# Kernel tuning notes

Hardware: AMD Instinct MI355X
Metric: run time of the kernel (lower is better)

The kernel has to match this reference:

```python
import jax, jax.numpy as jnp
import numpy as np

N_NODES = 50000
N_EDGES = 800000
IN_F = 128
HEADS = 4
OUT_F = 16  # per-head channels; concat output = HEADS*OUT_F = 64
NEG_SLOPE = 0.2


def setup_inputs() -> dict:
    key = jax.random.key(0)
    ks = jax.random.split(key, 9)
    x = jax.random.normal(ks[0], (N_NODES, IN_F), dtype=jnp.float32)
    edge_index = jax.random.randint(ks[1], (2, N_EDGES), 0, N_NODES, dtype=jnp.int64)
    edge_attr = jax.random.normal(ks[2], (N_EDGES, 1), dtype=jnp.float32)
    s = 1.0 / np.sqrt(IN_F)
    W = jax.random.normal(ks[3], (IN_F, HEADS * OUT_F), dtype=jnp.float32) * s
    W_edge = jax.random.normal(ks[4], (1, HEADS * OUT_F), dtype=jnp.float32)
    att_src = jax.random.normal(ks[5], (HEADS, OUT_F), dtype=jnp.float32) * s
    att_dst = jax.random.normal(ks[6], (HEADS, OUT_F), dtype=jnp.float32) * s
    att_edge = jax.random.normal(ks[7], (HEADS, OUT_F), dtype=jnp.float32) * s
    bias = jax.random.normal(ks[8], (HEADS * OUT_F,), dtype=jnp.float32) * 0.01
    return {"x": x, "edge_index": edge_index, "edge_attr": edge_attr,
            "W": W, "W_edge": W_edge, "att_src": att_src,
            "att_dst": att_dst, "att_edge": att_edge, "bias": bias}


def reference(x, edge_index, edge_attr, W, W_edge, att_src, att_dst, att_edge, bias):
    N = x.shape[0]
    H, C = att_src.shape
    src, dst = edge_index[0], edge_index[1]

    # add_self_loops with fill_value='mean': per-dst mean of incoming edge_attr
    deg = jax.ops.segment_sum(jnp.ones_like(edge_attr[:, 0]), dst, num_segments=N)
    ea_mean = jax.ops.segment_sum(edge_attr, dst, num_segments=N) / jnp.maximum(deg, 1.0)[:, None]
    loop = jnp.arange(N, dtype=src.dtype)
    src_f = jnp.concatenate([src, loop])   # [E+N]
    dst_f = jnp.concatenate([dst, loop])
    ea = jnp.concatenate([edge_attr, ea_mean], axis=0)  # [E+N, 1]

    # node transform + per-node attention logits
    xw = (x @ W).reshape(N, H, C)                 # [N,H,C]
    a_src = jnp.einsum('nhc,hc->nh', xw, att_src)  # [N,H]
    a_dst = jnp.einsum('nhc,hc->nh', xw, att_dst)

    # edge feature transform + edge logits
    ew = (ea @ W_edge).reshape(-1, H, C)           # [E+N,H,C]
    a_edge = jnp.einsum('ehc,hc->eh', ew, att_edge)

    # gather, LeakyReLU, segment softmax over incoming edges per dst node
    alpha = jax.nn.leaky_relu(a_src[src_f] + a_dst[dst_f] + a_edge, NEG_SLOPE)  # [E+N,H]
    amax = jax.ops.segment_max(alpha, dst_f, num_segments=N)                    # [N,H]
    ex = jnp.exp(alpha - amax[dst_f])
    denom = jax.ops.segment_sum(ex, dst_f, num_segments=N)
    att = ex / denom[dst_f]                                                     # [E+N,H]

    # weighted scatter-aggregate of source messages
    msg = xw[src_f] * att[:, :, None]                       # [E+N,H,C]
    out = jax.ops.segment_sum(msg, dst_f, num_segments=N)    # [N,H,C]
    out = out.reshape(N, H * C) + bias

    # batchnorm=Identity, dropout in eval mode; activation=relu
    return jax.nn.relu(out)
```

## Files before the change

### kernel.cpp

```cpp
#include <hip/hip_runtime.h>
#include <hip/hip_fp16.h>
#include <math.h>

#define NN 50000
#define NE 800000
#define INF_ 128
#define HEADS 4
#define OUTF 16
#define HC 64
#define NEG_SLOPE 0.2f
#define NBKT 196
#define CHA 4096
#define NBA ((NE + CHA - 1) / CHA)
#define XPAD 136

typedef _Float16 half8 __attribute__((ext_vector_type(8)));
typedef float f32x4 __attribute__((ext_vector_type(4)));

__device__ __forceinline__ unsigned short h2u(float f) {
    __half h = __float2half(f);
    return *(unsigned short*)&h;
}
__device__ __forceinline__ float u2f(unsigned short u) {
    __half h = *(__half*)&u;
    return __half2float(h);
}

__global__ __launch_bounds__(256) void k_xw(
    const float* __restrict__ x, const float* __restrict__ W,
    const float* __restrict__ att_src, const float* __restrict__ att_dst,
    unsigned short* __restrict__ xw16, unsigned short* __restrict__ a_src16,
    float* __restrict__ a_dst) {
    __shared__ _Float16 sxh[64][XPAD];
    __shared__ _Float16 sWT[64][XPAD];
    int t = threadIdx.x;
    int n0 = blockIdx.x * 64;
    for (int i = t; i < 64 * 32; i += 256) {
        int r = i >> 5, c4 = (i & 31) * 4;
        int n = n0 + r;
        float4 v = (n < NN) ? *(const float4*)&x[(size_t)n * INF_ + c4]
                            : make_float4(0.f, 0.f, 0.f, 0.f);
        sxh[r][c4 + 0] = (_Float16)v.x;
        sxh[r][c4 + 1] = (_Float16)v.y;
        sxh[r][c4 + 2] = (_Float16)v.z;
        sxh[r][c4 + 3] = (_Float16)v.w;
    }
    for (int i = t; i < INF_ * HC; i += 256) {
        int k = i >> 6, c = i & 63;
        sWT[c][k] = (_Float16)W[i];
    }
    __syncthreads();
    int w = t >> 6, l = t & 63;
    int lr = l & 15, kg = l >> 4;
    f32x4 acc0 = {0.f,0.f,0.f,0.f}, acc1 = acc0, acc2 = acc0, acc3 = acc0;
#pragma unroll
    for (int kk = 0; kk < 4; ++kk) {
        half8 a = *(half8*)&sxh[w * 16 + lr][kk * 32 + kg * 8];
        half8 b0 = *(half8*)&sWT[0 * 16 + lr][kk * 32 + kg * 8];
        half8 b1 = *(half8*)&sWT[1 * 16 + lr][kk * 32 + kg * 8];
        half8 b2 = *(half8*)&sWT[2 * 16 + lr][kk * 32 + kg * 8];
        half8 b3 = *(half8*)&sWT[3 * 16 + lr][kk * 32 + kg * 8];
        acc0 = __builtin_amdgcn_mfma_f32_16x16x32_f16(a, b0, acc0, 0, 0, 0);
        acc1 = __builtin_amdgcn_mfma_f32_16x16x32_f16(a, b1, acc1, 0, 0, 0);
        acc2 = __builtin_amdgcn_mfma_f32_16x16x32_f16(a, b2, acc2, 0, 0, 0);
        acc3 = __builtin_amdgcn_mfma_f32_16x16x32_f16(a, b3, acc3, 0, 0, 0);
    }
    float attS[4], attD[4];
#pragma unroll
    for (int ct = 0; ct < 4; ++ct) {
        attS[ct] = att_src[ct * 16 + lr];
        attD[ct] = att_dst[ct * 16 + lr];
    }
    int rbase = n0 + w * 16 + kg * 4;
    f32x4 accs[4] = {acc0, acc1, acc2, acc3};
#pragma unroll
    for (int ct = 0; ct < 4; ++ct) {
#pragma unroll
        for (int j = 0; j < 4; ++j) {
            float c = accs[ct][j];
            int node = rbase + j;
            if (node < NN)
                xw16[(size_t)node * HC + ct * 16 + lr] = h2u(c);
            float vs = c * attS[ct];
            float vd = c * attD[ct];
#pragma unroll
            for (int m = 1; m < 16; m <<= 1) {
                vs += __shfl_xor(vs, m);
                vd += __shfl_xor(vd, m);
            }
            if (lr == 0 && node < NN) {
                a_src16[node * HEADS + ct] = h2u(vs);
                a_dst[node * HEADS + ct] = vd;
            }
        }
    }
}

__global__ __launch_bounds__(256) void k_coarse(const int* __restrict__ ei,
                                                int* __restrict__ ccnt) {
    __shared__ int lh[NBKT];
    int t = threadIdx.x;
    for (int i = t; i < NBKT; i += 256) lh[i] = 0;
    __syncthreads();
    for (int i = blockIdx.x * 256 + t; i < NE; i += gridDim.x * 256)
        atomicAdd(&lh[ei[NE + i] >> 8], 1);
    __syncthreads();
    for (int i = t; i < NBKT; i += 256)
        if (lh[i]) atomicAdd(&ccnt[i], lh[i]);
}

__global__ void k_scanb(const int* __restrict__ ccnt, int* __restrict__ boff,
                        int* __restrict__ ccur) {
    __shared__ int sd[256];
    int t = threadIdx.x;
    int v = (t < NBKT) ? ccnt[t] : 0;
    sd[t] = v; __syncthreads();
    for (int o = 1; o < 256; o <<= 1) {
        int a = (t >= o) ? sd[t - o] : 0;
        __syncthreads();
        sd[t] += a;
        __syncthreads();
    }
    int ex = sd[t] - v;
    if (t < NBKT) { boff[t] = ex; ccur[t] = ex; }
    if (t == NBKT - 1) boff[NBKT] = sd[t];
}

__global__ __launch_bounds__(256) void k_binA(const int* __restrict__ ei,
                                              const float* __restrict__ ea,
                                              int* __restrict__ ccur,
                                              uint2* __restrict__ ebuf) {
    __shared__ int lh[NBKT], lcur[NBKT];
    int t = threadIdx.x;
    int e0 = blockIdx.x * CHA;
    int ecnt = NE - e0; if (ecnt > CHA) ecnt = CHA;
    for (int i = t; i < NBKT; i += 256) lh[i] = 0;
    __syncthreads();
    int dloc[16];
    int nj = 0;
    for (int i = t; i < ecnt; i += 256, ++nj) {
        int dst = ei[NE + e0 + i];
        dloc[nj] = dst;
        atomicAdd(&lh[dst >> 8], 1);
    }
    __syncthreads();
    for (int i = t; i < NBKT; i += 256)
        lcur[i] = lh[i] ? atomicAdd(&ccur[i], lh[i]) : 0;
    __syncthreads();
    nj = 0;
    for (int i = t; i < ecnt; i += 256, ++nj) {
        int e = e0 + i;
        int dst = dloc[nj];
        int p = atomicAdd(&lcur[dst >> 8], 1);
        uint2 pk;
        pk.x = (unsigned)ei[e] | ((unsigned)(dst & 255) << 16);
        pk.y = __float_as_uint(ea[e]);
        ebuf[p] = pk;
    }
}

__global__ __launch_bounds__(256) void k_binB(const int* __restrict__ boff,
                                              const uint2* __restrict__ ebuf,
                                              uint2* __restrict__ esort,
                                              int* __restrict__ deg,
                                              int* __restrict__ offs,
                                              float* __restrict__ easum) {
    __shared__ int lh[256], lcur[256], sd[256];
    __shared__ float lsum[256];
    int t = threadIdx.x;
    int b = blockIdx.x;
    int base = boff[b];
    int cnt = boff[b + 1] - base;
    lh[t] = 0;
    lsum[t] = 0.f;
    __syncthreads();
    for (int i = t; i < cnt; i += 256)
        atomicAdd(&lh[(ebuf[base + i].x >> 16) & 255], 1);
    __syncthreads();
    int v = lh[t];
    sd[t] = v; __syncthreads();
    for (int o = 1; o < 256; o <<= 1) {
        int a = (t >= o) ? sd[t - o] : 0;
        __syncthreads();
        sd[t] += a;
        __syncthreads();
    }
    int ex = sd[t] - v;
    lcur[t] = ex;
    __syncthreads();
    for (int i = t; i < cnt; i += 256) {
        uint2 pk = ebuf[base + i];
        int d = (pk.x >> 16) & 255;
        int p = atomicAdd(&lcur[d], 1);
        atomicAdd(&lsum[d], __uint_as_float(pk.y));
        esort[base + p] = make_uint2(pk.x & 0xFFFFu, pk.y);
    }
    __syncthreads();
    int n = (b << 8) + t;
    if (n < NN) { deg[n] = v; offs[n] = base + ex; easum[n] = lsum[t]; }
}

__device__ __forceinline__ float lrelu(float v) {
    return v > 0.f ? v : NEG_SLOPE * v;
}

__global__ __launch_bounds__(256) void k_gather(
    const uint2* __restrict__ esort, const int* __restrict__ offs,
    const int* __restrict__ deg, const float* __restrict__ easum,
    const unsigned short* __restrict__ a_src16, const float* __restrict__ a_dst,
    const unsigned short* __restrict__ xw16,
    const float* __restrict__ W_edge, const float* __restrict__ att_edge,
    const float* __restrict__ bias, float* __restrict__ out) {
    __shared__ __align__(16) float sce[4];
    int t = threadIdx.x;
    if (t < 4) {
        float s_ = 0.f;
        for (int k = 0; k < OUTF; ++k)
            s_ = fmaf(W_edge[t * OUTF + k], att_edge[t * OUTF + k], s_);
        sce[t] = s_;
    }
    __syncthreads();
    int lane = t & 63;
    int wslot = t >> 6;
    int n = (blockIdx.x << 2) + wslot;
    int e16 = lane & 15, hA = lane >> 4;
    int l32 = lane & 31, g = lane >> 5;
    int c2 = l32 * 2, h2 = l32 >> 3;

    float ceA = sce[hA];
    float adA = a_dst[n * HEADS + hA];
    int start = offs[n];
    int cnt = deg[n];

    float mA = -3e38f, mB = -3e38f;
    float s = 0.f, a0 = 0.f, a1 = 0.f;

    int nch = (cnt + 15) >> 4;
    for (int ch = 0; ch < nch; ++ch) {
        int base = start + (ch << 4);
        int cc = cnt - (ch << 4); if (cc > 16) cc = 16;
        bool valid = e16 < cc;
        uint2 pk = esort[base + e16];
        int srci = (int)(pk.x & 0xFFFFu);
        float eav = __uint_as_float(pk.y);
        float asv = u2f(a_src16[srci * HEADS + hA]);
        float lg = -3e38f;
        if (valid) lg = lrelu(asv + adA + eav * ceA);
        float cm = lg;
#pragma unroll
        for (int mm = 1; mm < 16; mm <<= 1) cm = fmaxf(cm, __shfl_xor(cm, mm));
        float mA2 = fmaxf(mA, cm);
        float p = __expf(lg - mA2);
        mA = mA2;
        float cmB = __shfl(cm, h2 << 4);
        float mB2 = fmaxf(mB, cmB);
        float r = __expf(mB - mB2);
        s *= r; a0 *= r; a1 *= r;
        mB = mB2;
        int iters = (cc + 1) & ~1;
#pragma unroll 4
        for (int i = 0; i < iters; i += 2) {
            int ii = i + g;
            float pv = __shfl(p, (h2 << 4) | ii);
            int si = __shfl(srci, ii);
            if (ii < cc) {
                unsigned xv = *(const unsigned*)&xw16[(size_t)si * HC + c2];
                float x0 = u2f((unsigned short)(xv & 0xFFFFu));
                float x1 = u2f((unsigned short)(xv >> 16));
                s += pv;
                a0 = fmaf(pv, x0, a0);
                a1 = fmaf(pv, x1, a1);
            }
        }
    }
    s  += __shfl_xor(s, 32);
    a0 += __shfl_xor(a0, 32);
    a1 += __shfl_xor(a1, 32);
    float ceB = sce[h2];
    float adB = a_dst[n * HEADS + h2];
    float asnB = u2f(a_src16[n * HEADS + h2]);
    float eavm = easum[n] / fmaxf((float)cnt, 1.f);
    float al = lrelu(asnB + adB + eavm * ceB);
    float mn = fmaxf(mB, al);
    float r = __expf(mB - mn);
    float pp = __expf(al - mn);
    unsigned xs = *(const unsigned*)&xw16[(size_t)n * HC + c2];
    s = s * r + pp;
    a0 = a0 * r + pp * u2f((unsigned short)(xs & 0xFFFFu));
    a1 = a1 * r + pp * u2f((unsigned short)(xs >> 16));
    if (g == 0) {
        float2 o;
        o.x = fmaxf(a0 / s + bias[c2], 0.f);
        o.y = fmaxf(a1 / s + bias[c2 + 1], 0.f);
        *(float2*)&out[(size_t)n * HC + c2] = o;
    }
}

extern "C" void kernel_launch(void* const* d_in, const int* in_sizes, int n_in,
                              void* d_out, int out_size, void* d_ws, size_t ws_size,
                              hipStream_t stream) {
    const float* x        = (const float*)d_in[0];
    const int*   ei       = (const int*)d_in[1];
    const float* ea       = (const float*)d_in[2];
    const float* W        = (const float*)d_in[3];
    const float* W_edge   = (const float*)d_in[4];
    const float* att_src  = (const float*)d_in[5];
    const float* att_dst  = (const float*)d_in[6];
    const float* att_edge = (const float*)d_in[7];
    const float* bias     = (const float*)d_in[8];
    float* out = (float*)d_out;

    float* ws = (float*)d_ws;
    unsigned short* xw16    = (unsigned short*)ws;
    uint2* esort  = (uint2*)(ws + (size_t)32 * NN);
    uint2* ebuf   = esort + NE;
    unsigned short* a_src16 = (unsigned short*)(ebuf + NE);
    float* a_dst  = (float*)(a_src16 + (size_t)HEADS * NN);
    int*   deg    = (int*)(a_dst + (size_t)HEADS * NN);
    int*   offs   = deg + NN;
    float* easum  = (float*)(offs + NN);
    int*   ccnt   = (int*)(easum + NN);
    int*   ccur   = ccnt + NBKT;
    int*   boff   = ccur + NBKT;

    hipMemsetAsync(ccnt, 0, NBKT * sizeof(int), stream);
    k_coarse<<<256, 256, 0, stream>>>(ei, ccnt);
    k_scanb<<<1, 256, 0, stream>>>(ccnt, boff, ccur);
    k_binA<<<NBA, 256, 0, stream>>>(ei, ea, ccur, ebuf);
    k_binB<<<NBKT, 256, 0, stream>>>(boff, ebuf, esort, deg, offs, easum);
    k_xw<<<(NN + 63) / 64, 256, 0, stream>>>(x, W, att_src, att_dst, xw16, a_src16, a_dst);
    k_gather<<<NN / 4, 256, 0, stream>>>(
        esort, offs, deg, easum, a_src16, a_dst, xw16, W_edge, att_edge, bias, out);
}
```

Measured before the change: 189.3 us.

## Fuse fine bucket sort into gather kernel using LDS-local edge sort per 64-node bucket

Coarse buckets shrink from 256 to 64 destination nodes, and the second binning kernel is removed. The gather kernel now sorts each bucket's edges in shared memory and computes the per-node mean edge attribute itself. It also replaces online max-tracked softmax with a direct exp (no max subtraction) and stages probabilities and sources through LDS instead of shuffles. This removes a full pass over edge buffers and extra global writes. The costs are fp16 edge attributes, possible exp overflow without max subtraction, and fewer blocks (782) each processing 64 nodes serially across 4 waves.

Measured after the change: 209.5 us. 10.7% more time.

```diff
diff --git a/kernel.cpp b/kernel.cpp
--- a/kernel.cpp
+++ b/kernel.cpp
@@ -9,9 +9,10 @@
 #define OUTF 16
 #define HC 64
 #define NEG_SLOPE 0.2f
-#define NBKT 196
+#define NBKT2 ((NN + 63) >> 6)
 #define CHA 4096
 #define NBA ((NE + CHA - 1) / CHA)
+#define CAPE 2048
 #define XPAD 136
 
 typedef _Float16 half8 __attribute__((ext_vector_type(8)));
@@ -24,6 +25,9 @@
 __device__ __forceinline__ float u2f(unsigned short u) {
     __half h = *(__half*)&u;
     return __half2float(h);
+}
+__device__ __forceinline__ float lrelu(float v) {
+    return v > 0.f ? v : NEG_SLOPE * v;
 }
 
 __global__ __launch_bounds__(256) void k_xw(
@@ -98,14 +102,14 @@
 
 __global__ __launch_bounds__(256) void k_coarse(const int* __restrict__ ei,
                                                 int* __restrict__ ccnt) {
-    __shared__ int lh[NBKT];
+    __shared__ int lh[NBKT2];
     int t = threadIdx.x;
-    for (int i = t; i < NBKT; i += 256) lh[i] = 0;
+    for (int i = t; i < NBKT2; i += 256) lh[i] = 0;
     __syncthreads();
     for (int i = blockIdx.x * 256 + t; i < NE; i += gridDim.x * 256)
-        atomicAdd(&lh[ei[NE + i] >> 8], 1);
+        atomicAdd(&lh[ei[NE + i] >> 6], 1);
     __syncthreads();
-    for (int i = t; i < NBKT; i += 256)
+    for (int i = t; i < NBKT2; i += 256)
         if (lh[i]) atomicAdd(&ccnt[i], lh[i]);
 }
 
@@ -113,105 +117,90 @@
                         int* __restrict__ ccur) {
     __shared__ int sd[256];
     int t = threadIdx.x;
-    int v = (t < NBKT) ? ccnt[t] : 0;
-    sd[t] = v; __syncthreads();
+    int b4 = t * 4;
+    int c[4], pre[4];
+#pragma unroll
+    for (int j = 0; j < 4; ++j)
+        c[j] = (b4 + j < NBKT2) ? ccnt[b4 + j] : 0;
+    pre[0] = 0;
+#pragma unroll
+    for (int j = 1; j < 4; ++j) pre[j] = pre[j - 1] + c[j - 1];
+    int tot = pre[3] + c[3];
+    sd[t] = tot; __syncthreads();
     for (int o = 1; o < 256; o <<= 1) {
         int a = (t >= o) ? sd[t - o] : 0;
         __syncthreads();
         sd[t] += a;
         __syncthreads();
     }
-    int ex = sd[t] - v;
-    if (t < NBKT) { boff[t] = ex; ccur[t] = ex; }
-    if (t == NBKT - 1) boff[NBKT] = sd[t];
+    int ex = sd[t] - tot;
+#pragma unroll
+    for (int j = 0; j < 4; ++j)
+        if (b4 + j < NBKT2) { boff[b4 + j] = ex + pre[j]; ccur[b4 + j] = ex + pre[j]; }
+    if (t == 255) boff[NBKT2] = sd[255];
 }
 
 __global__ __launch_bounds__(256) void k_binA(const int* __restrict__ ei,
                                               const float* __restrict__ ea,
                                               int* __restrict__ ccur,
                                               uint2* __restrict__ ebuf) {
-    __shared__ int lh[NBKT], lcur[NBKT];
+    __shared__ int lh[NBKT2], lcur[NBKT2];
     int t = threadIdx.x;
     int e0 = blockIdx.x * CHA;
     int ecnt = NE - e0; if (ecnt > CHA) ecnt = CHA;
-    for (int i = t; i < NBKT; i += 256) lh[i] = 0;
+    for (int i = t; i < NBKT2; i += 256) lh[i] = 0;
     __syncthreads();
-    int dloc[16];
-    int nj = 0;
-    for (int i = t; i < ecnt; i += 256, ++nj) {
-        int dst = ei[NE + e0 + i];
-        dloc[nj] = dst;
-        atomicAdd(&lh[dst >> 8], 1);
-    }
-    __syncthreads();
-    for (int i = t; i < NBKT; i += 256)
-        lcur[i] = lh[i] ? atomicAdd(&ccur[i], lh[i]) : 0;
-    __syncthreads();
-    nj = 0;
-    for (int i = t; i < ecnt; i += 256, ++nj) {
-        int e = e0 + i;
-        int dst = dloc[nj];
-        int p = atomicAdd(&lcur[dst >> 8], 1);
-        uint2 pk;
-        pk.x = (unsigned)ei[e] | ((unsigned)(dst & 255) << 16);
-        pk.y = __float_as_uint(ea[e]);
-        ebuf[p] = pk;
-    }
-}
-
-__global__ __launch_bounds__(256) void k_binB(const int* __restrict__ boff,
-                                              const uint2* __restrict__ ebuf,
-                                              uint2* __restrict__ esort,
-                                              int* __restrict__ deg,
-                                              int* __restrict__ offs,
-                                              float* __restrict__ easum) {
-    __shared__ int lh[256], lcur[256], sd[256];
-    __shared__ float lsum[256];
-    int t = threadIdx.x;
-    int b = blockIdx.x;
-    int base = boff[b];
-    int cnt = boff[b + 1] - base;
-    lh[t] = 0;
-    lsum[t] = 0.f;
-    __syncthreads();
-    for (int i = t; i < cnt; i += 256)
-        atomicAdd(&lh[(ebuf[base + i].x >> 16) & 255], 1);
-    __syncthreads();
-    int v = lh[t];
-    sd[t] = v; __syncthreads();
-    for (int o = 1; o < 256; o <<= 1) {
-        int a = (t >= o) ? sd[t - o] : 0;
-        __syncthreads();
-        sd[t] += a;
-        __syncthreads();
-    }
-    int ex = sd[t] - v;
-    lcur[t] = ex;
-    __syncthreads();
-    for (int i = t; i < cnt; i += 256) {
-        uint2 pk = ebuf[base + i];
-        int d = (pk.x >> 16) & 255;
-        int p = atomicAdd(&lcur[d], 1);
-        atomicAdd(&lsum[d], __uint_as_float(pk.y));
-        esort[base + p] = make_uint2(pk.x & 0xFFFFu, pk.y);
-    }
-    __syncthreads();
-    int n = (b << 8) + t;
-    if (n < NN) { deg[n] = v; offs[n] = base + ex; easum[n] = lsum[t]; }
-}
-
-__device__ __forceinline__ float lrelu(float v) {
-    return v > 0.f ? v : NEG_SLOPE * v;
-}
-
-__global__ __launch_bounds__(256) void k_gather(
-    const uint2* __restrict__ esort, const int* __restrict__ offs,
-    const int* __restrict__ deg, const float* __restrict__ easum,
+    if (ecnt == CHA) {
+        int dl[16];
+#pragma unroll
+        for (int j = 0; j < 16; ++j) {
+            dl[j] = ei[NE + e0 + t + j * 256];
+            atomicAdd(&lh[dl[j] >> 6], 1);
+        }
+        __syncthreads();
+        for (int i = t; i < NBKT2; i += 256)
+            lcur[i] = lh[i] ? atomicAdd(&ccur[i], lh[i]) : 0;
+        __syncthreads();
+#pragma unroll
+        for (int j = 0; j < 16; ++j) {
+            int e = e0 + t + j * 256;
+            int dst = dl[j];
+            int p = atomicAdd(&lcur[dst >> 6], 1);
+            uint2 pk;
+            pk.x = (unsigned)ei[e] | ((unsigned)(dst & 63) << 16);
+            pk.y = __float_as_uint(ea[e]);
+            ebuf[p] = pk;
+        }
+    } else {
+        for (int i = t; i < ecnt; i += 256)
+            atomicAdd(&lh[ei[NE + e0 + i] >> 6], 1);
+        __syncthreads();
+        for (int i = t; i < NBKT2; i += 256)
+            lcur[i] = lh[i] ? atomicAdd(&ccur[i], lh[i]) : 0;
+        __syncthreads();
+        for (int i = t; i < ecnt; i += 256) {
+            int e = e0 + i;
+            int dst = ei[NE + e];
+            int p = atomicAdd(&lcur[dst >> 6], 1);
+            uint2 pk;
+            pk.x = (unsigned)ei[e] | ((unsigned)(dst & 63) << 16);
+            pk.y = __float_as_uint(ea[e]);
+            ebuf[p] = pk;
+        }
+    }
+}
+
+__global__ __launch_bounds__(256) void k_gfuse(
+    const int* __restrict__ boff, const uint2* __restrict__ ebuf,
     const unsigned short* __restrict__ a_src16, const float* __restrict__ a_dst,
     const unsigned short* __restrict__ xw16,
     const float* __restrict__ W_edge, const float* __restrict__ att_edge,
     const float* __restrict__ bias, float* __restrict__ out) {
     __shared__ __align__(16) float sce[4];
+    __shared__ unsigned sedge[CAPE + 16];
+    __shared__ int lh[64], lofs[64], lcur[64];
+    __shared__ __align__(16) float ldsP[4][16][4];
+    __shared__ int ldsS[4][16];
     int t = threadIdx.x;
     if (t < 4) {
         float s_ = 0.f;
@@ -219,80 +208,178 @@
             s_ = fmaf(W_edge[t * OUTF + k], att_edge[t * OUTF + k], s_);
         sce[t] = s_;
     }
+    if (t < 64) lh[t] = 0;
     __syncthreads();
-    int lane = t & 63;
-    int wslot = t >> 6;
-    int n = (blockIdx.x << 2) + wslot;
+
+    int b = blockIdx.x;
+    int base = boff[b];
+    int cntb = boff[b + 1] - base;
+    int w = t >> 6, lane = t & 63;
     int e16 = lane & 15, hA = lane >> 4;
     int l32 = lane & 31, g = lane >> 5;
     int c2 = l32 * 2, h2 = l32 >> 3;
-
     float ceA = sce[hA];
-    float adA = a_dst[n * HEADS + hA];
-    int start = offs[n];
-    int cnt = deg[n];
-
-    float mA = -3e38f, mB = -3e38f;
-    float s = 0.f, a0 = 0.f, a1 = 0.f;
-
-    int nch = (cnt + 15) >> 4;
-    for (int ch = 0; ch < nch; ++ch) {
-        int base = start + (ch << 4);
-        int cc = cnt - (ch << 4); if (cc > 16) cc = 16;
-        bool valid = e16 < cc;
-        uint2 pk = esort[base + e16];
-        int srci = (int)(pk.x & 0xFFFFu);
-        float eav = __uint_as_float(pk.y);
-        float asv = u2f(a_src16[srci * HEADS + hA]);
-        float lg = -3e38f;
-        if (valid) lg = lrelu(asv + adA + eav * ceA);
-        float cm = lg;
-#pragma unroll
-        for (int mm = 1; mm < 16; mm <<= 1) cm = fmaxf(cm, __shfl_xor(cm, mm));
-        float mA2 = fmaxf(mA, cm);
-        float p = __expf(lg - mA2);
-        mA = mA2;
-        float cmB = __shfl(cm, h2 << 4);
-        float mB2 = fmaxf(mB, cmB);
-        float r = __expf(mB - mB2);
-        s *= r; a0 *= r; a1 *= r;
-        mB = mB2;
-        int iters = (cc + 1) & ~1;
+
+    if (cntb <= CAPE) {
+        uint2 held[8];
+#pragma unroll
+        for (int j = 0; j < 8; ++j) {
+            int i = t + j * 256;
+            if (i < cntb) {
+                held[j] = ebuf[base + i];
+                atomicAdd(&lh[held[j].x >> 16], 1);
+            }
+        }
+        __syncthreads();
+        if (t < 64) {
+            int v = lh[t], xx = v;
+#pragma unroll
+            for (int o = 1; o < 64; o <<= 1) {
+                int nn_ = __shfl_up(xx, o);
+                if (lane >= o) xx += nn_;
+            }
+            lofs[t] = xx - v; lcur[t] = xx - v;
+        }
+        __syncthreads();
+#pragma unroll
+        for (int j = 0; j < 8; ++j) {
+            int i = t + j * 256;
+            if (i < cntb) {
+                uint2 pk = held[j];
+                int d = pk.x >> 16;
+                int p = atomicAdd(&lcur[d], 1);
+                sedge[p] = (pk.x & 0xFFFFu) |
+                           ((unsigned)h2u(__uint_as_float(pk.y)) << 16);
+            }
+        }
+        __syncthreads();
+        for (int q = 0; q < 16; ++q) {
+            int dl_ = (w << 4) + q;
+            int n = (b << 6) + dl_;
+            if (n >= NN) continue;
+            int rs = lofs[dl_], rl = lh[dl_];
+            float adA = a_dst[n * 4 + hA];
+            float s = 0.f, a0 = 0.f, a1 = 0.f, easum = 0.f;
+            int nch = (rl + 15) >> 4;
+            for (int ch = 0; ch < nch; ++ch) {
+                int cbase = rs + (ch << 4);
+                int cc = rl - (ch << 4); if (cc > 16) cc = 16;
+                bool valid = e16 < cc;
+                unsigned se = sedge[cbase + e16];
+                int srci = se & 0xFFFFu;
+                float eav = u2f((unsigned short)(se >> 16));
+                float asv = u2f(a_src16[srci * 4 + hA]);
+                float p = 0.f, es = 0.f;
+                if (valid) {
+                    p = __expf(lrelu(asv + adA + eav * ceA));
+                    es = eav;
+                }
+#pragma unroll
+                for (int mm = 1; mm < 16; mm <<= 1) es += __shfl_xor(es, mm);
+                easum += es;
+                ldsP[w][e16][hA] = p;
+                if (hA == 0) ldsS[w][e16] = srci;
+                asm volatile("s_waitcnt lgkmcnt(0)" ::: "memory");
+                __builtin_amdgcn_sched_barrier(0);
 #pragma unroll 4
-        for (int i = 0; i < iters; i += 2) {
-            int ii = i + g;
-            float pv = __shfl(p, (h2 << 4) | ii);
-            int si = __shfl(srci, ii);
-            if (ii < cc) {
-                unsigned xv = *(const unsigned*)&xw16[(size_t)si * HC + c2];
-                float x0 = u2f((unsigned short)(xv & 0xFFFFu));
-                float x1 = u2f((unsigned short)(xv >> 16));
-                s += pv;
-                a0 = fmaf(pv, x0, a0);
-                a1 = fmaf(pv, x1, a1);
-            }
-        }
-    }
-    s  += __shfl_xor(s, 32);
-    a0 += __shfl_xor(a0, 32);
-    a1 += __shfl_xor(a1, 32);
-    float ceB = sce[h2];
-    float adB = a_dst[n * HEADS + h2];
-    float asnB = u2f(a_src16[n * HEADS + h2]);
-    float eavm = easum[n] / fmaxf((float)cnt, 1.f);
-    float al = lrelu(asnB + adB + eavm * ceB);
-    float mn = fmaxf(mB, al);
-    float r = __expf(mB - mn);
-    float pp = __expf(al - mn);
-    unsigned xs = *(const unsigned*)&xw16[(size_t)n * HC + c2];
-    s = s * r + pp;
-    a0 = a0 * r + pp * u2f((unsigned short)(xs & 0xFFFFu));
-    a1 = a1 * r + pp * u2f((unsigned short)(xs >> 16));
-    if (g == 0) {
-        float2 o;
-        o.x = fmaxf(a0 / s + bias[c2], 0.f);
-        o.y = fmaxf(a1 / s + bias[c2 + 1], 0.f);
-        *(float2*)&out[(size_t)n * HC + c2] = o;
+                for (int i = 0; i < cc; i += 2) {
+                    int ii = i + g;
+                    if (ii < cc) {
+                        float pv = ldsP[w][ii][h2];
+                        int si = ldsS[w][ii];
+                        unsigned xv = *(const unsigned*)&xw16[(size_t)si * HC + c2];
+                        s += pv;
+                        a0 = fmaf(pv, u2f((unsigned short)(xv & 0xFFFFu)), a0);
+                        a1 = fmaf(pv, u2f((unsigned short)(xv >> 16)), a1);
+                    }
+                }
+                asm volatile("s_waitcnt lgkmcnt(0)" ::: "memory");
+                __builtin_amdgcn_sched_barrier(0);
+            }
+            s  += __shfl_xor(s, 32);
+            a0 += __shfl_xor(a0, 32);
+            a1 += __shfl_xor(a1, 32);
+            float adB = a_dst[n * 4 + h2];
+            float asnB = u2f(a_src16[n * 4 + h2]);
+            float eavm = easum / fmaxf((float)rl, 1.f);
+            float pp = __expf(lrelu(asnB + adB + eavm * sce[h2]));
+            unsigned xs = *(const unsigned*)&xw16[(size_t)n * HC + c2];
+            s += pp;
+            a0 = fmaf(pp, u2f((unsigned short)(xs & 0xFFFFu)), a0);
+            a1 = fmaf(pp, u2f((unsigned short)(xs >> 16)), a1);
+            if (g == 0) {
+                float2 o;
+                o.x = fmaxf(a0 / s + bias[c2], 0.f);
+                o.y = fmaxf(a1 / s + bias[c2 + 1], 0.f);
+                *(float2*)&out[(size_t)n * HC + c2] = o;
+            }
+        }
+    } else {
+        for (int q = 0; q < 16; ++q) {
+            int dl_ = (w << 4) + q;
+            int n = (b << 6) + dl_;
+            if (n >= NN) continue;
+            float adA = a_dst[n * 4 + hA];
+            float s = 0.f, a0 = 0.f, a1 = 0.f, easum = 0.f;
+            int deg = 0;
+            int nch = (cntb + 15) >> 4;
+            for (int ch = 0; ch < nch; ++ch) {
+                int cbase = base + (ch << 4);
+                int cc = cntb - (ch << 4); if (cc > 16) cc = 16;
+                bool valid = e16 < cc;
+                uint2 pk = valid ? ebuf[cbase + e16] : make_uint2(0u, 0u);
+                bool mine = valid && ((int)(pk.x >> 16) == dl_);
+                int srci = pk.x & 0xFFFFu;
+                float eav = __uint_as_float(pk.y);
+                float asv = u2f(a_src16[srci * 4 + hA]);
+                float p = 0.f, es = 0.f; int dd = 0;
+                if (mine) {
+                    p = __expf(lrelu(asv + adA + eav * ceA));
+                    es = eav; dd = 1;
+                }
+#pragma unroll
+                for (int mm = 1; mm < 16; mm <<= 1) {
+                    es += __shfl_xor(es, mm);
+                    dd += __shfl_xor(dd, mm);
+                }
+                easum += es; deg += dd;
+                ldsP[w][e16][hA] = p;
+                if (hA == 0) ldsS[w][e16] = srci;
+                asm volatile("s_waitcnt lgkmcnt(0)" ::: "memory");
+                __builtin_amdgcn_sched_barrier(0);
+#pragma unroll 4
+                for (int i = 0; i < cc; i += 2) {
+                    int ii = i + g;
+                    if (ii < cc) {
+                        float pv = ldsP[w][ii][h2];
+                        int si = ldsS[w][ii];
+                        unsigned xv = *(const unsigned*)&xw16[(size_t)si * HC + c2];
+                        s += pv;
+                        a0 = fmaf(pv, u2f((unsigned short)(xv & 0xFFFFu)), a0);
+                        a1 = fmaf(pv, u2f((unsigned short)(xv >> 16)), a1);
+                    }
+                }
+                asm volatile("s_waitcnt lgkmcnt(0)" ::: "memory");
+                __builtin_amdgcn_sched_barrier(0);
+            }
+            s  += __shfl_xor(s, 32);
+            a0 += __shfl_xor(a0, 32);
+            a1 += __shfl_xor(a1, 32);
+            float adB = a_dst[n * 4 + h2];
+            float asnB = u2f(a_src16[n * 4 + h2]);
+            float eavm = easum / fmaxf((float)deg, 1.f);
+            float pp = __expf(lrelu(asnB + adB + eavm * sce[h2]));
+            unsigned xs = *(const unsigned*)&xw16[(size_t)n * HC + c2];
+            s += pp;
+            a0 = fmaf(pp, u2f((unsigned short)(xs & 0xFFFFu)), a0);
+            a1 = fmaf(pp, u2f((unsigned short)(xs >> 16)), a1);
+            if (g == 0) {
+                float2 o;
+                o.x = fmaxf(a0 / s + bias[c2], 0.f);
+                o.y = fmaxf(a1 / s + bias[c2 + 1], 0.f);
+                *(float2*)&out[(size_t)n * HC + c2] = o;
+            }
+        }
     }
 }
 
@@ -312,23 +399,18 @@
 
     float* ws = (float*)d_ws;
     unsigned short* xw16    = (unsigned short*)ws;
-    uint2* esort  = (uint2*)(ws + (size_t)32 * NN);
-    uint2* ebuf   = esort + NE;
+    uint2* ebuf   = (uint2*)(ws + (size_t)32 * NN);
     unsigned short* a_src16 = (unsigned short*)(ebuf + NE);
     float* a_dst  = (float*)(a_src16 + (size_t)HEADS * NN);
-    int*   deg    = (int*)(a_dst + (size_t)HEADS * NN);
-    int*   offs   = deg + NN;
-    float* easum  = (float*)(offs + NN);
-    int*   ccnt   = (int*)(easum + NN);
-    int*   ccur   = ccnt + NBKT;
-    int*   boff   = ccur + NBKT;
-
-    hipMemsetAsync(ccnt, 0, NBKT * sizeof(int), stream);
+    int*   ccnt   = (int*)(a_dst + (size_t)HEADS * NN);
+    int*   ccur   = ccnt + NBKT2;
+    int*   boff   = ccur + NBKT2;
+
+    hipMemsetAsync(ccnt, 0, NBKT2 * sizeof(int), stream);
     k_coarse<<<256, 256, 0, stream>>>(ei, ccnt);
     k_scanb<<<1, 256, 0, stream>>>(ccnt, boff, ccur);
     k_binA<<<NBA, 256, 0, stream>>>(ei, ea, ccur, ebuf);
-    k_binB<<<NBKT, 256, 0, stream>>>(boff, ebuf, esort, deg, offs, easum);
     k_xw<<<(NN + 63) / 64, 256, 0, stream>>>(x, W, att_src, att_dst, xw16, a_src16, a_dst);
-    k_gather<<<NN / 4, 256, 0, stream>>>(
-        esort, offs, deg, easum, a_src16, a_dst, xw16, W_edge, att_edge, bias, out);
-}
+    k_gfuse<<<NBKT2, 256, 0, stream>>>(
+        boff, ebuf, a_src16, a_dst, xw16, W_edge, att_edge, bias, out);
+}
```
